# Performance work log

Hardware: AMD Instinct MI355X
Metric: run time of the kernel (lower is better)

Reference implementation:

```python
import jax, jax.numpy as jnp
import numpy as np

N, C, W_DIM, H_DIM = 2, 256, 64, 64
HEADS = 4
DH = C // HEADS  # per-head dim for Q,K,V projections
EPS = 1e-5


def _layernorm(x, w, b):
    mu = jnp.mean(x, axis=-1, keepdims=True)
    var = jnp.var(x, axis=-1, keepdims=True)
    return (x - mu) * jax.lax.rsqrt(var + EPS) * w + b


def setup_inputs() -> dict:
    key = jax.random.key(0)
    ks = jax.random.split(key, 12)
    s = 1.0 / np.sqrt(C)
    return {
        "x": jax.random.normal(ks[0], (N, C, W_DIM, H_DIM), dtype=jnp.float32),
        "ln1_w": jnp.ones((C,), jnp.float32),
        "ln1_b": jnp.zeros((C,), jnp.float32),
        # per-head projection weights, laid out for x @ W: [heads, C, DH]
        "WQ": jax.random.normal(ks[1], (HEADS, C, DH), jnp.float32) * s,
        "WK": jax.random.normal(ks[2], (HEADS, C, DH), jnp.float32) * s,
        "WV": jax.random.normal(ks[3], (HEADS, C, DH), jnp.float32) * s,
        "ln2_w": jnp.ones((C,), jnp.float32),
        "ln2_b": jnp.zeros((C,), jnp.float32),
        "W1": jax.random.normal(ks[4], (C, C), jnp.float32) * s,
        "b1": jnp.zeros((C,), jnp.float32),
        "W2": jax.random.normal(ks[5], (C, C), jnp.float32) * s,
        "b2": jnp.zeros((C,), jnp.float32),
    }


def reference(x, ln1_w, ln1_b, WQ, WK, WV, ln2_w, ln2_b, W1, b1, W2, b2):
    n, c, w, h = x.shape
    s = w * h
    # 'n c w h -> n (w h) c'
    r = x.reshape(n, c, s).transpose(0, 2, 1)          # [n, s, c]
    norm = _layernorm(r, ln1_w, ln1_b)
    # all heads at once (original loops over heads)
    Q = jnp.einsum('nsc,hcd->nhsd', norm, WQ)
    K = jnp.einsum('nsc,hcd->nhsd', norm, WK)
    V = jnp.einsum('nsc,hcd->nhsd', norm, WV)
    # scale is 1/sqrt(seq_len) per original (keys.shape[1])
    y = jnp.einsum('nhqd,nhkd->nhqk', Q, K) / jnp.sqrt(jnp.float32(s))
    # QUIRK: softmax over dim=1 of [n, q, k] => the QUERY axis (axis=2 here)
    z = jax.nn.softmax(y, axis=2)
    attn = jnp.einsum('nhqk,nhkd->nhqd', z, V)         # [n, h, s, dh]
    attn_cat = attn.transpose(0, 2, 1, 3).reshape(n, s, c)
    out = attn_cat + r
    out = _layernorm(out, ln2_w, ln2_b)
    out = jax.nn.gelu(out @ W1 + b1, approximate=False) @ W2 + b2
    out = out + attn_cat
    # 'n (w h) c -> n c w h'
    return out.transpose(0, 2, 1).reshape(n, c, w, h)
```

## Files before the change

### kernel.cpp

```cpp
#include <hip/hip_runtime.h>
#include <math.h>

#define SEQ 4096
#define CH  256
#define NHT 8
#define DHD 64

#define QSCALE 0.0225421092f

using bf16x8 = __attribute__((ext_vector_type(8))) short;
using f32x4  = __attribute__((ext_vector_type(4))) float;
typedef unsigned short u16;
typedef unsigned int   u32;

__device__ __forceinline__ u16 f2bf(float f) {
    u32 u = __float_as_uint(f);
    u = (u + 0x7fffu + ((u >> 16) & 1u)) >> 16;
    return (u16)u;
}
__device__ __forceinline__ float bf2f(u16 h) {
    return __uint_as_float(((u32)h) << 16);
}
__device__ __forceinline__ float fexp2(float x) {
    return __builtin_amdgcn_exp2f(x);
}

__global__ __launch_bounds__(256) void k_prep(const float* __restrict__ x,
                                              const float* __restrict__ ln1w,
                                              const float* __restrict__ ln1b,
                                              const float* __restrict__ WQ,
                                              const float* __restrict__ WK,
                                              const float* __restrict__ WV,
                                              const float* __restrict__ W1,
                                              const float* __restrict__ W2,
                                              u16* __restrict__ norm,
                                              u16* __restrict__ BtQKV,
                                              u16* __restrict__ W1t,
                                              u16* __restrict__ W2t)
{
    __shared__ float tile[32][257];
    __shared__ float mu[32], rs[32];
    int bid = blockIdx.x;
    int t = threadIdx.x;
    if (bid < 1280) {
        int id = bid * 256 + t;
        if (id < 768 * 256) {
            int j = id >> 8, c = id & 255;
            int which = j >> 8, h = (j >> 6) & 3, d = j & 63;
            const float* W = (which == 0) ? WQ : (which == 1) ? WK : WV;
            BtQKV[id] = f2bf(W[(h * 256 + c) * 64 + d]);
        } else if (id < 768 * 256 + 65536) {
            int jj = id - 768 * 256;
            int j = jj >> 8, c = jj & 255;
            W1t[jj] = f2bf(W1[c * 256 + j]);
        } else if (id < 768 * 256 + 2 * 65536) {
            int jj = id - 768 * 256 - 65536;
            int j = jj >> 8, c = jj & 255;
            W2t[jj] = f2bf(W2[c * 256 + j]);
        }
        return;
    }
    int b2i = bid - 1280;
    int n = b2i >> 7, s0 = (b2i & 127) * 32;
    int sl = t & 31, cg = t >> 5;
    for (int cc = 0; cc < 256; cc += 8) {
        int c = cc + cg;
        tile[sl][c] = x[(n * 256 + c) * SEQ + s0 + sl];
    }
    __syncthreads();
    int wv = t >> 6, l = t & 63;
    for (int rr = 0; rr < 8; rr++) {
        int s = wv * 8 + rr;
        float a0 = tile[s][l], a1 = tile[s][l + 64], a2 = tile[s][l + 128], a3 = tile[s][l + 192];
        float sm = a0 + a1 + a2 + a3;
        float sq = a0 * a0 + a1 * a1 + a2 * a2 + a3 * a3;
        for (int off = 32; off; off >>= 1) { sm += __shfl_xor(sm, off); sq += __shfl_xor(sq, off); }
        if (l == 0) {
            float m = sm * (1.f / 256.f);
            mu[s] = m;
            rs[s] = rsqrtf(sq * (1.f / 256.f) - m * m + 1e-5f);
        }
    }
    __syncthreads();
    float ww = ln1w[t], bb = ln1b[t];
    for (int s = 0; s < 32; s++) {
        float v = (tile[s][t] - mu[s]) * rs[s] * ww + bb;
        norm[(n * SEQ + s0 + s) * 256 + t] = f2bf(v);
    }
}

__global__ __launch_bounds__(256) void k_qkv(const u16* __restrict__ norm,
                                             const u16* __restrict__ Bt,
                                             u16* __restrict__ Qo,
                                             u16* __restrict__ Ko,
                                             u16* __restrict__ Vo)
{
    int m0 = blockIdx.x * 64, j0 = blockIdx.y * 128;
    int t = threadIdx.x, w = t >> 6, lane = t & 63, quad = lane >> 4, l16 = lane & 15;
    const u16* Ap = norm + (long)(m0 + w * 16 + l16) * 256;
    const u16* Bp = Bt + (long)j0 * 256;
    f32x4 z = {0.f, 0.f, 0.f, 0.f};
    f32x4 acc[8];
    #pragma unroll
    for (int j = 0; j < 8; j++) acc[j] = z;
    #pragma unroll
    for (int kc = 0; kc < 8; kc++) {
        bf16x8 a = *(const bf16x8*)&Ap[kc * 32 + quad * 8];
        #pragma unroll
        for (int j = 0; j < 8; j++) {
            bf16x8 b = *(const bf16x8*)&Bp[(long)(j * 16 + l16) * 256 + kc * 32 + quad * 8];
            acc[j] = __builtin_amdgcn_mfma_f32_16x16x32_bf16(a, b, acc[j], 0, 0, 0);
        }
    }
    #pragma unroll
    for (int j = 0; j < 8; j++) {
        int col = j0 + j * 16 + l16;
        int which = col >> 8, h = (col >> 6) & 3, d = col & 63;
        u16* dst = (which == 0) ? Qo : (which == 1) ? Ko : Vo;
        float sc = (which == 0) ? QSCALE : 1.0f;
        #pragma unroll
        for (int r = 0; r < 4; r++) {
            int m = m0 + w * 16 + quad * 4 + r;
            int n = m >> 12, s = m & 4095;
            dst[((n * 4 + h) * SEQ + s) * 64 + d] = f2bf(acc[j][r] * sc);
        }
    }
}

__global__ __launch_bounds__(256) void k_pass1(const u16* __restrict__ Q,
                                               const u16* __restrict__ Km,
                                               float* __restrict__ D4)
{
    __shared__ float Dred[128];
    int nh = blockIdx.y, k0 = blockIdx.x * 128, qc = blockIdx.z;
    const u16* Qh = Q + (long)nh * SEQ * 64;
    const u16* Kh = Km + (long)nh * SEQ * 64;
    int t = threadIdx.x, w = t >> 6, lane = t & 63, quad = lane >> 4, l16 = lane & 15;
    bf16x8 Kf[8][2];
    #pragma unroll
    for (int i = 0; i < 8; i++) {
        Kf[i][0] = *(const bf16x8*)&Kh[(k0 + i * 16 + l16) * 64 + quad * 8];
        Kf[i][1] = *(const bf16x8*)&Kh[(k0 + i * 16 + l16) * 64 + 32 + quad * 8];
    }
    if (t < 128) Dred[t] = 0.f;
    f32x4 z = {0.f, 0.f, 0.f, 0.f};
    float Dacc[8][4] = {};
    const int qw0 = qc * 1024 + w * 256;
    bf16x8 b0 = *(const bf16x8*)&Qh[(qw0 + l16) * 64 + quad * 8];
    bf16x8 b1 = *(const bf16x8*)&Qh[(qw0 + l16) * 64 + 32 + quad * 8];
    for (int step = 0; step < 16; step++) {
        int q = qw0 + step * 16;
        bf16x8 n0, n1;
        if (step < 15) {
            n0 = *(const bf16x8*)&Qh[(q + 16 + l16) * 64 + quad * 8];
            n1 = *(const bf16x8*)&Qh[(q + 16 + l16) * 64 + 32 + quad * 8];
        }
        #pragma unroll
        for (int i = 0; i < 8; i++) {
            f32x4 acc = z;
            acc = __builtin_amdgcn_mfma_f32_16x16x32_bf16(Kf[i][0], b0, acc, 0, 0, 0);
            acc = __builtin_amdgcn_mfma_f32_16x16x32_bf16(Kf[i][1], b1, acc, 0, 0, 0);
            #pragma unroll
            for (int r = 0; r < 4; r++) Dacc[i][r] += fexp2(acc[r]);
        }
        b0 = n0; b1 = n1;
    }
    #pragma unroll
    for (int i = 0; i < 8; i++)
        #pragma unroll
        for (int r = 0; r < 4; r++) {
            float v = Dacc[i][r];
            v += __shfl_xor(v, 1); v += __shfl_xor(v, 2);
            v += __shfl_xor(v, 4); v += __shfl_xor(v, 8);
            Dacc[i][r] = v;
        }
    __syncthreads();
    if (l16 == 0) {
        #pragma unroll
        for (int i = 0; i < 8; i++)
            #pragma unroll
            for (int r = 0; r < 4; r++)
                atomicAdd(&Dred[i * 16 + quad * 4 + r], Dacc[i][r]);
    }
    __syncthreads();
    if (t < 128) D4[((long)(qc * NHT + nh)) * SEQ + k0 + t] = Dred[t];
}

__global__ __launch_bounds__(256) void k_scaleV(const u16* __restrict__ V,
                                                const float* __restrict__ D4,
                                                u16* __restrict__ Vt)
{
    __shared__ float tile[64][65];
    int nh = blockIdx.y, k0 = blockIdx.x * 64;
    int t = threadIdx.x;
    int d = t & 63, kk = t >> 6;
    const u16* Vh = V + (long)nh * SEQ * 64;
    for (int p = 0; p < 16; p++) {
        int k = p * 4 + kk;
        float Dv = D4[((long)(0 * NHT + nh)) * SEQ + k0 + k]
                 + D4[((long)(1 * NHT + nh)) * SEQ + k0 + k]
                 + D4[((long)(2 * NHT + nh)) * SEQ + k0 + k]
                 + D4[((long)(3 * NHT + nh)) * SEQ + k0 + k];
        tile[k][d] = bf2f(Vh[(k0 + k) * 64 + d]) * (1.f / Dv);
    }
    __syncthreads();
    int k2 = t & 63, d4 = t >> 6;
    u16* Vth = Vt + (long)nh * 64 * SEQ;
    for (int p = 0; p < 16; p++) {
        int dd = p * 4 + d4;
        Vth[dd * SEQ + k0 + k2] = f2bf(tile[k2][dd]);
    }
}

__global__ __launch_bounds__(256) void k_pass2(const u16* __restrict__ Q,
                                               const u16* __restrict__ Km,
                                               const u16* __restrict__ Vt,
                                               float* __restrict__ acat2)
{
    __shared__ __align__(16) unsigned char smem[34816];
    u16 (*lP)[64][36] = (u16(*)[64][36])smem;
    float (*SA)[68] = (float(*)[68])smem;
    float (*SB)[68] = (float(*)[68])(smem + 17408);

    int nh = blockIdx.y, q0 = blockIdx.x * 64, kcid = blockIdx.z;
    int n = nh >> 2, h = nh & 3;
    const u16* Qh = Q + (long)nh * SEQ * 64;
    const u16* Kh = Km + (long)nh * SEQ * 64;
    const u16* Vh = Vt + (long)nh * 64 * SEQ;
    int t = threadIdx.x, w = t >> 6, lane = t & 63, quad = lane >> 4, l16 = lane & 15;
    bf16x8 Qf[4][2];
    #pragma unroll
    for (int jq = 0; jq < 4; jq++)
        #pragma unroll
        for (int ch = 0; ch < 2; ch++)
            Qf[jq][ch] = *(const bf16x8*)&Qh[(q0 + jq * 16 + l16) * 64 + ch * 32 + quad * 8];
    f32x4 z = {0.f, 0.f, 0.f, 0.f};
    f32x4 accO[4][4];
    #pragma unroll
    for (int jq = 0; jq < 4; jq++)
        #pragma unroll
        for (int jd = 0; jd < 4; jd++) accO[jq][jd] = z;

    const int kw0 = kcid * 2048 + w * 512;
    bf16x8 kA[2][2], nA[2][2];
    #pragma unroll
    for (int ksub = 0; ksub < 2; ksub++) {
        kA[ksub][0] = *(const bf16x8*)&Kh[(kw0 + ksub * 16 + l16) * 64 + quad * 8];
        kA[ksub][1] = *(const bf16x8*)&Kh[(kw0 + ksub * 16 + l16) * 64 + 32 + quad * 8];
    }
    for (int step = 0; step < 16; step++) {
        int k0 = kw0 + step * 32;
        if (step < 15) {
            #pragma unroll
            for (int ksub = 0; ksub < 2; ksub++) {
                nA[ksub][0] = *(const bf16x8*)&Kh[(k0 + 32 + ksub * 16 + l16) * 64 + quad * 8];
                nA[ksub][1] = *(const bf16x8*)&Kh[(k0 + 32 + ksub * 16 + l16) * 64 + 32 + quad * 8];
            }
        }
        #pragma unroll
        for (int ksub = 0; ksub < 2; ksub++) {
            #pragma unroll
            for (int jq = 0; jq < 4; jq++) {
                f32x4 acc = z;
                acc = __builtin_amdgcn_mfma_f32_16x16x32_bf16(kA[ksub][0], Qf[jq][0], acc, 0, 0, 0);
                acc = __builtin_amdgcn_mfma_f32_16x16x32_bf16(kA[ksub][1], Qf[jq][1], acc, 0, 0, 0);
                u32 e0 = __float_as_uint(fexp2(acc[0]));
                u32 e1 = __float_as_uint(fexp2(acc[1]));
                u32 e2 = __float_as_uint(fexp2(acc[2]));
                u32 e3 = __float_as_uint(fexp2(acc[3]));
                uint2 pk;
                pk.x = __builtin_amdgcn_perm(e1, e0, 0x07060302u);
                pk.y = __builtin_amdgcn_perm(e3, e2, 0x07060302u);
                *(uint2*)&lP[w][jq * 16 + l16][ksub * 16 + quad * 4] = pk;
            }
        }
        #pragma unroll
        for (int jq = 0; jq < 4; jq++) {
            bf16x8 pa = *(const bf16x8*)&lP[w][jq * 16 + l16][quad * 8];
            #pragma unroll
            for (int jd = 0; jd < 4; jd++) {
                bf16x8 vb = *(const bf16x8*)&Vh[(jd * 16 + l16) * SEQ + k0 + quad * 8];
                accO[jq][jd] = __builtin_amdgcn_mfma_f32_16x16x32_bf16(pa, vb, accO[jq][jd], 0, 0, 0);
            }
        }
        #pragma unroll
        for (int ksub = 0; ksub < 2; ksub++) {
            kA[ksub][0] = nA[ksub][0];
            kA[ksub][1] = nA[ksub][1];
        }
    }
    __syncthreads();
    if (w >= 2) {
        float (*S)[68] = (w == 2) ? SA : SB;
        #pragma unroll
        for (int jq = 0; jq < 4; jq++)
            #pragma unroll
            for (int jd = 0; jd < 4; jd++)
                #pragma unroll
                for (int r = 0; r < 4; r++)
                    S[jq * 16 + quad * 4 + r][jd * 16 + l16] = accO[jq][jd][r];
    }
    __syncthreads();
    if (w < 2) {
        float (*S)[68] = (w == 0) ? SA : SB;
        #pragma unroll
        for (int jq = 0; jq < 4; jq++)
            #pragma unroll
            for (int jd = 0; jd < 4; jd++)
                #pragma unroll
                for (int r = 0; r < 4; r++) {
                    float v = accO[jq][jd][r] + S[jq * 16 + quad * 4 + r][jd * 16 + l16];
                    S[jq * 16 + quad * 4 + r][jd * 16 + l16] = v;
                }
    }
    __syncthreads();
    float* dst = acat2 + (long)kcid * 8192 * 256;
    #pragma unroll
    for (int p = 0; p < 4; p++) {
        int row = p * 16 + (t >> 4);
        int ch = (t & 15) * 4;
        float4 va = *(float4*)&SA[row][ch];
        float4 vb = *(float4*)&SB[row][ch];
        float4 o = make_float4(va.x + vb.x, va.y + vb.y, va.z + vb.z, va.w + vb.w);
        *(float4*)&dst[((long)n * SEQ + q0 + row) * 256 + h * 64 + ch] = o;
    }
}

__global__ __launch_bounds__(256) void k_tail(const float* __restrict__ x,
                                              const float* __restrict__ acat2,
                                              const float* __restrict__ lnw,
                                              const float* __restrict__ lnb,
                                              const u16* __restrict__ W1t,
                                              const float* __restrict__ b1v,
                                              const u16* __restrict__ W2t,
                                              const float* __restrict__ b2v,
                                              float* __restrict__ out)
{
    __shared__ __align__(16) unsigned char smem[16448];
    float (*tile)[257] = (float(*)[257])smem;
    u16 (*lT)[264] = (u16(*)[264])smem;
    __shared__ float mu[16], rs[16];
    __shared__ __align__(16) u16 lH[16][264];

    const long STRIDE = (long)8192 * 256;
    int m0 = blockIdx.x * 16;
    int n = m0 >> 12, s0 = m0 & 4095;
    int t = threadIdx.x, w = t >> 6, lane = t & 63, quad = lane >> 4, l16 = lane & 15;

    {
        int sl = t & 15, cg = t >> 4;
        for (int cc = 0; cc < 256; cc += 16) {
            int c = cc + cg;
            tile[sl][c] = x[(n * 256 + c) * SEQ + s0 + sl];
        }
    }
    __syncthreads();
    for (int s = 0; s < 16; s++) {
        long idx = (long)(m0 + s) * 256 + t;
        tile[s][t] += acat2[idx] + acat2[idx + STRIDE];
    }
    __syncthreads();
    {
        int l = t & 63;
        for (int rr = 0; rr < 4; rr++) {
            int s = w * 4 + rr;
            float a0 = tile[s][l], a1 = tile[s][l + 64], a2 = tile[s][l + 128], a3 = tile[s][l + 192];
            float sm = a0 + a1 + a2 + a3;
            float sq = a0 * a0 + a1 * a1 + a2 * a2 + a3 * a3;
            for (int off = 32; off; off >>= 1) { sm += __shfl_xor(sm, off); sq += __shfl_xor(sq, off); }
            if (l == 0) {
                float m = sm * (1.f / 256.f);
                mu[s] = m;
                rs[s] = rsqrtf(sq * (1.f / 256.f) - m * m + 1e-5f);
            }
        }
    }
    __syncthreads();
    {
        float ww = lnw[t], bb = lnb[t];
        for (int s = 0; s < 16; s++)
            lH[s][t] = f2bf((tile[s][t] - mu[s]) * rs[s] * ww + bb);
    }
    __syncthreads();

    f32x4 z = {0.f, 0.f, 0.f, 0.f};
    f32x4 acc1[4];
    #pragma unroll
    for (int js = 0; js < 4; js++) acc1[js] = z;
    #pragma unroll
    for (int kc = 0; kc < 8; kc++) {
        bf16x8 b = *(const bf16x8*)&lH[l16][kc * 32 + quad * 8];
        #pragma unroll
        for (int js = 0; js < 4; js++) {
            bf16x8 a = *(const bf16x8*)&W1t[(long)(w * 64 + js * 16 + l16) * 256 + kc * 32 + quad * 8];
            acc1[js] = __builtin_amdgcn_mfma_f32_16x16x32_bf16(a, b, acc1[js], 0, 0, 0);
        }
    }
    #pragma unroll
    for (int js = 0; js < 4; js++) {
        u32 e[4];
        #pragma unroll
        for (int r = 0; r < 4; r++) {
            int j = w * 64 + js * 16 + quad * 4 + r;
            float v = acc1[js][r] + b1v[j];
            float g = 0.5f * v * (1.f + erff(v * 0.70710678118f));
            u32 u = __float_as_uint(g);
            e[r] = u + 0x7fffu + ((u >> 16) & 1u);
        }
        uint2 pk;
        pk.x = __builtin_amdgcn_perm(e[1], e[0], 0x07060302u);
        pk.y = __builtin_amdgcn_perm(e[3], e[2], 0x07060302u);
        *(uint2*)&lT[l16][w * 64 + js * 16 + quad * 4] = pk;
    }
    __syncthreads();
    f32x4 acc2[4];
    #pragma unroll
    for (int cs = 0; cs < 4; cs++) acc2[cs] = z;
    #pragma unroll
    for (int kc = 0; kc < 8; kc++) {
        bf16x8 pa = *(const bf16x8*)&lT[l16][kc * 32 + quad * 8];
        #pragma unroll
        for (int cs = 0; cs < 4; cs++) {
            bf16x8 wb = *(const bf16x8*)&W2t[(long)(w * 64 + cs * 16 + l16) * 256 + kc * 32 + quad * 8];
            acc2[cs] = __builtin_amdgcn_mfma_f32_16x16x32_bf16(pa, wb, acc2[cs], 0, 0, 0);
        }
    }
    #pragma unroll
    for (int cs = 0; cs < 4; cs++) {
        int c = w * 64 + cs * 16 + l16;
        float bj = b2v[c];
        float vv[4];
        #pragma unroll
        for (int r = 0; r < 4; r++) {
            long idx = (long)(m0 + quad * 4 + r) * 256 + c;
            vv[r] = acc2[cs][r] + bj + acat2[idx] + acat2[idx + STRIDE];
        }
        float4 o = make_float4(vv[0], vv[1], vv[2], vv[3]);
        *(float4*)&out[((long)n * 256 + c) * SEQ + s0 + quad * 4] = o;
    }
}

extern "C" void kernel_launch(void* const* d_in, const int* in_sizes, int n_in,
                              void* d_out, int out_size, void* d_ws, size_t ws_size,
                              hipStream_t stream) {
    const float* x    = (const float*)d_in[0];
    const float* ln1w = (const float*)d_in[1];
    const float* ln1b = (const float*)d_in[2];
    const float* WQ   = (const float*)d_in[3];
    const float* WK   = (const float*)d_in[4];
    const float* WV   = (const float*)d_in[5];
    const float* ln2w = (const float*)d_in[6];
    const float* ln2b = (const float*)d_in[7];
    const float* W1   = (const float*)d_in[8];
    const float* b1   = (const float*)d_in[9];
    const float* W2   = (const float*)d_in[10];
    const float* b2   = (const float*)d_in[11];
    float* out = (float*)d_out;

    char* p = (char*)d_ws;
    u16* norm   = (u16*)p;   p += (size_t)8192 * 256 * 2;
    u16* BtQKV  = (u16*)p;   p += (size_t)768 * 256 * 2;
    u16* W1t    = (u16*)p;   p += (size_t)256 * 256 * 2;
    u16* W2t    = (u16*)p;   p += (size_t)256 * 256 * 2;
    u16* Qb     = (u16*)p;   p += (size_t)NHT * SEQ * 64 * 2;
    u16* Kb     = (u16*)p;   p += (size_t)NHT * SEQ * 64 * 2;
    u16* Vb     = (u16*)p;   p += (size_t)NHT * SEQ * 64 * 2;
    float* D4   = (float*)p; p += (size_t)4 * NHT * SEQ * 4;
    u16* Vt     = (u16*)p;   p += (size_t)NHT * SEQ * 64 * 2;
    float* acat2= (float*)p; p += (size_t)2 * 8192 * 256 * 4;

    k_prep<<<1536, 256, 0, stream>>>(x, ln1w, ln1b, WQ, WK, WV, W1, W2,
                                     norm, BtQKV, W1t, W2t);
    k_qkv<<<dim3(128, 6), 256, 0, stream>>>(norm, BtQKV, Qb, Kb, Vb);
    k_pass1<<<dim3(32, 8, 4), 256, 0, stream>>>(Qb, Kb, D4);
    k_scaleV<<<dim3(64, 8), 256, 0, stream>>>(Vb, D4, Vt);
    k_pass2<<<dim3(64, 8, 2), 256, 0, stream>>>(Qb, Kb, Vt, acat2);
    k_tail<<<512, 256, 0, stream>>>(x, acat2, ln2w, ln2b, W1t, b1, W2t, b2, out);
}
```

Before: 257.6 us.

## Fold softmax normalization into pass2 exponent and write V transposed from QKV

Removes the k_scaleV kernel. The QKV GEMM now writes V directly in transposed [d][seq] layout. pass2 loads the per-key column sums into LDS as log2 values and subtracts them inside the exponent, so the normalization no longer multiplies V. pass2 is also restructured to software-pipeline the QK exponentials into registers one step ahead and to prefetch the V fragments. The aim is to save a kernel launch and a full read/write of V. The cost is extra LDS traffic and register pressure in pass2, and the change in rounding (bf16 V no longer pre-scaled).

```diff
diff --git a/kernel.cpp b/kernel.cpp
--- a/kernel.cpp
+++ b/kernel.cpp
@@ -93,7 +93,7 @@
                                              const u16* __restrict__ Bt,
                                              u16* __restrict__ Qo,
                                              u16* __restrict__ Ko,
-                                             u16* __restrict__ Vo)
+                                             u16* __restrict__ Vto)
 {
     int m0 = blockIdx.x * 64, j0 = blockIdx.y * 128;
     int t = threadIdx.x, w = t >> 6, lane = t & 63, quad = lane >> 4, l16 = lane & 15;
@@ -116,13 +116,21 @@
     for (int j = 0; j < 8; j++) {
         int col = j0 + j * 16 + l16;
         int which = col >> 8, h = (col >> 6) & 3, d = col & 63;
-        u16* dst = (which == 0) ? Qo : (which == 1) ? Ko : Vo;
-        float sc = (which == 0) ? QSCALE : 1.0f;
-        #pragma unroll
-        for (int r = 0; r < 4; r++) {
-            int m = m0 + w * 16 + quad * 4 + r;
-            int n = m >> 12, s = m & 4095;
-            dst[((n * 4 + h) * SEQ + s) * 64 + d] = f2bf(acc[j][r] * sc);
+        int m = m0 + w * 16 + quad * 4;
+        int n = m >> 12, s = m & 4095;
+        if (which == 2) {
+            u16 h0 = f2bf(acc[j][0]), h1 = f2bf(acc[j][1]);
+            u16 h2_ = f2bf(acc[j][2]), h3 = f2bf(acc[j][3]);
+            uint2 pk;
+            pk.x = (u32)h0 | ((u32)h1 << 16);
+            pk.y = (u32)h2_ | ((u32)h3 << 16);
+            *(uint2*)&Vto[((long)(n * 4 + h) * 64 + d) * SEQ + s] = pk;
+        } else {
+            u16* dst = (which == 0) ? Qo : Ko;
+            float sc = (which == 0) ? QSCALE : 1.0f;
+            #pragma unroll
+            for (int r = 0; r < 4; r++)
+                dst[((n * 4 + h) * SEQ + s + r) * 64 + d] = f2bf(acc[j][r] * sc);
         }
     }
 }
@@ -186,39 +194,15 @@
     if (t < 128) D4[((long)(qc * NHT + nh)) * SEQ + k0 + t] = Dred[t];
 }
 
-__global__ __launch_bounds__(256) void k_scaleV(const u16* __restrict__ V,
-                                                const float* __restrict__ D4,
-                                                u16* __restrict__ Vt)
-{
-    __shared__ float tile[64][65];
-    int nh = blockIdx.y, k0 = blockIdx.x * 64;
-    int t = threadIdx.x;
-    int d = t & 63, kk = t >> 6;
-    const u16* Vh = V + (long)nh * SEQ * 64;
-    for (int p = 0; p < 16; p++) {
-        int k = p * 4 + kk;
-        float Dv = D4[((long)(0 * NHT + nh)) * SEQ + k0 + k]
-                 + D4[((long)(1 * NHT + nh)) * SEQ + k0 + k]
-                 + D4[((long)(2 * NHT + nh)) * SEQ + k0 + k]
-                 + D4[((long)(3 * NHT + nh)) * SEQ + k0 + k];
-        tile[k][d] = bf2f(Vh[(k0 + k) * 64 + d]) * (1.f / Dv);
-    }
-    __syncthreads();
-    int k2 = t & 63, d4 = t >> 6;
-    u16* Vth = Vt + (long)nh * 64 * SEQ;
-    for (int p = 0; p < 16; p++) {
-        int dd = p * 4 + d4;
-        Vth[dd * SEQ + k0 + k2] = f2bf(tile[k2][dd]);
-    }
-}
-
 __global__ __launch_bounds__(256) void k_pass2(const u16* __restrict__ Q,
                                                const u16* __restrict__ Km,
                                                const u16* __restrict__ Vt,
+                                               const float* __restrict__ D4,
                                                float* __restrict__ acat2)
 {
     __shared__ __align__(16) unsigned char smem[34816];
     u16 (*lP)[64][36] = (u16(*)[64][36])smem;
+    float* Lk = (float*)(smem + 18432);
     float (*SA)[68] = (float(*)[68])smem;
     float (*SB)[68] = (float(*)[68])(smem + 17408);
 
@@ -228,65 +212,115 @@
     const u16* Kh = Km + (long)nh * SEQ * 64;
     const u16* Vh = Vt + (long)nh * 64 * SEQ;
     int t = threadIdx.x, w = t >> 6, lane = t & 63, quad = lane >> 4, l16 = lane & 15;
+    const int kw0 = kcid * 2048 + w * 512;
+    const int klw = w * 512;
+
+    {
+        const float* Dp = D4 + (long)nh * SEQ + kcid * 2048;
+        const long QS = (long)NHT * SEQ;
+        #pragma unroll
+        for (int off = 0; off < 8; off++) {
+            int kl = off * 256 + t;
+            float s = Dp[kl] + Dp[QS + kl] + Dp[2 * QS + kl] + Dp[3 * QS + kl];
+            Lk[kl] = __log2f(s);
+        }
+    }
     bf16x8 Qf[4][2];
     #pragma unroll
     for (int jq = 0; jq < 4; jq++)
         #pragma unroll
         for (int ch = 0; ch < 2; ch++)
             Qf[jq][ch] = *(const bf16x8*)&Qh[(q0 + jq * 16 + l16) * 64 + ch * 32 + quad * 8];
-    f32x4 z = {0.f, 0.f, 0.f, 0.f};
-    f32x4 accO[4][4];
-    #pragma unroll
-    for (int jq = 0; jq < 4; jq++)
-        #pragma unroll
-        for (int jd = 0; jd < 4; jd++) accO[jq][jd] = z;
-
-    const int kw0 = kcid * 2048 + w * 512;
-    bf16x8 kA[2][2], nA[2][2];
+    bf16x8 kA[2][2];
     #pragma unroll
     for (int ksub = 0; ksub < 2; ksub++) {
         kA[ksub][0] = *(const bf16x8*)&Kh[(kw0 + ksub * 16 + l16) * 64 + quad * 8];
         kA[ksub][1] = *(const bf16x8*)&Kh[(kw0 + ksub * 16 + l16) * 64 + 32 + quad * 8];
     }
-    for (int step = 0; step < 16; step++) {
-        int k0 = kw0 + step * 32;
-        if (step < 15) {
-            #pragma unroll
-            for (int ksub = 0; ksub < 2; ksub++) {
-                nA[ksub][0] = *(const bf16x8*)&Kh[(k0 + 32 + ksub * 16 + l16) * 64 + quad * 8];
-                nA[ksub][1] = *(const bf16x8*)&Kh[(k0 + 32 + ksub * 16 + l16) * 64 + 32 + quad * 8];
-            }
-        }
-        #pragma unroll
-        for (int ksub = 0; ksub < 2; ksub++) {
+    f32x4 z = {0.f, 0.f, 0.f, 0.f};
+    f32x4 accO[4][4];
+    #pragma unroll
+    for (int jq = 0; jq < 4; jq++)
+        #pragma unroll
+        for (int jd = 0; jd < 4; jd++) accO[jq][jd] = z;
+    __syncthreads();
+
+    uint2 pk[2][4];
+    {
+        f32x4 Lv[2];
+        #pragma unroll
+        for (int ksub = 0; ksub < 2; ksub++)
+            Lv[ksub] = *(const f32x4*)&Lk[klw + ksub * 16 + quad * 4];
+        #pragma unroll
+        for (int ksub = 0; ksub < 2; ksub++)
             #pragma unroll
             for (int jq = 0; jq < 4; jq++) {
                 f32x4 acc = z;
                 acc = __builtin_amdgcn_mfma_f32_16x16x32_bf16(kA[ksub][0], Qf[jq][0], acc, 0, 0, 0);
                 acc = __builtin_amdgcn_mfma_f32_16x16x32_bf16(kA[ksub][1], Qf[jq][1], acc, 0, 0, 0);
-                u32 e0 = __float_as_uint(fexp2(acc[0]));
-                u32 e1 = __float_as_uint(fexp2(acc[1]));
-                u32 e2 = __float_as_uint(fexp2(acc[2]));
-                u32 e3 = __float_as_uint(fexp2(acc[3]));
-                uint2 pk;
-                pk.x = __builtin_amdgcn_perm(e1, e0, 0x07060302u);
-                pk.y = __builtin_amdgcn_perm(e3, e2, 0x07060302u);
-                *(uint2*)&lP[w][jq * 16 + l16][ksub * 16 + quad * 4] = pk;
+                u32 e0 = __float_as_uint(fexp2(acc[0] - Lv[ksub][0]));
+                u32 e1 = __float_as_uint(fexp2(acc[1] - Lv[ksub][1]));
+                u32 e2 = __float_as_uint(fexp2(acc[2] - Lv[ksub][2]));
+                u32 e3 = __float_as_uint(fexp2(acc[3] - Lv[ksub][3]));
+                pk[ksub][jq].x = __builtin_amdgcn_perm(e1, e0, 0x07060302u);
+                pk[ksub][jq].y = __builtin_amdgcn_perm(e3, e2, 0x07060302u);
+            }
+    }
+    #pragma unroll
+    for (int ksub = 0; ksub < 2; ksub++) {
+        kA[ksub][0] = *(const bf16x8*)&Kh[(kw0 + 32 + ksub * 16 + l16) * 64 + quad * 8];
+        kA[ksub][1] = *(const bf16x8*)&Kh[(kw0 + 32 + ksub * 16 + l16) * 64 + 32 + quad * 8];
+    }
+    bf16x8 vb[4];
+    #pragma unroll
+    for (int jd = 0; jd < 4; jd++)
+        vb[jd] = *(const bf16x8*)&Vh[(jd * 16 + l16) * SEQ + kw0 + quad * 8];
+
+    for (int i = 0; i < 16; i++) {
+        int k0 = kw0 + i * 32;
+        #pragma unroll
+        for (int ksub = 0; ksub < 2; ksub++)
+            #pragma unroll
+            for (int jq = 0; jq < 4; jq++)
+                *(uint2*)&lP[w][jq * 16 + l16][ksub * 16 + quad * 4] = pk[ksub][jq];
+        if (i < 15) {
+            f32x4 Lv[2];
+            #pragma unroll
+            for (int ksub = 0; ksub < 2; ksub++)
+                Lv[ksub] = *(const f32x4*)&Lk[klw + (i + 1) * 32 + ksub * 16 + quad * 4];
+            #pragma unroll
+            for (int ksub = 0; ksub < 2; ksub++)
+                #pragma unroll
+                for (int jq = 0; jq < 4; jq++) {
+                    f32x4 acc = z;
+                    acc = __builtin_amdgcn_mfma_f32_16x16x32_bf16(kA[ksub][0], Qf[jq][0], acc, 0, 0, 0);
+                    acc = __builtin_amdgcn_mfma_f32_16x16x32_bf16(kA[ksub][1], Qf[jq][1], acc, 0, 0, 0);
+                    u32 e0 = __float_as_uint(fexp2(acc[0] - Lv[ksub][0]));
+                    u32 e1 = __float_as_uint(fexp2(acc[1] - Lv[ksub][1]));
+                    u32 e2 = __float_as_uint(fexp2(acc[2] - Lv[ksub][2]));
+                    u32 e3 = __float_as_uint(fexp2(acc[3] - Lv[ksub][3]));
+                    pk[ksub][jq].x = __builtin_amdgcn_perm(e1, e0, 0x07060302u);
+                    pk[ksub][jq].y = __builtin_amdgcn_perm(e3, e2, 0x07060302u);
+                }
+            if (i < 14) {
+                #pragma unroll
+                for (int ksub = 0; ksub < 2; ksub++) {
+                    kA[ksub][0] = *(const bf16x8*)&Kh[(k0 + 64 + ksub * 16 + l16) * 64 + quad * 8];
+                    kA[ksub][1] = *(const bf16x8*)&Kh[(k0 + 64 + ksub * 16 + l16) * 64 + 32 + quad * 8];
+                }
             }
         }
         #pragma unroll
         for (int jq = 0; jq < 4; jq++) {
             bf16x8 pa = *(const bf16x8*)&lP[w][jq * 16 + l16][quad * 8];
             #pragma unroll
-            for (int jd = 0; jd < 4; jd++) {
-                bf16x8 vb = *(const bf16x8*)&Vh[(jd * 16 + l16) * SEQ + k0 + quad * 8];
-                accO[jq][jd] = __builtin_amdgcn_mfma_f32_16x16x32_bf16(pa, vb, accO[jq][jd], 0, 0, 0);
-            }
-        }
-        #pragma unroll
-        for (int ksub = 0; ksub < 2; ksub++) {
-            kA[ksub][0] = nA[ksub][0];
-            kA[ksub][1] = nA[ksub][1];
+            for (int jd = 0; jd < 4; jd++)
+                accO[jq][jd] = __builtin_amdgcn_mfma_f32_16x16x32_bf16(pa, vb[jd], accO[jq][jd], 0, 0, 0);
+        }
+        if (i < 15) {
+            #pragma unroll
+            for (int jd = 0; jd < 4; jd++)
+                vb[jd] = *(const bf16x8*)&Vh[(jd * 16 + l16) * SEQ + k0 + 32 + quad * 8];
         }
     }
     __syncthreads();
@@ -320,8 +354,8 @@
         int row = p * 16 + (t >> 4);
         int ch = (t & 15) * 4;
         float4 va = *(float4*)&SA[row][ch];
-        float4 vb = *(float4*)&SB[row][ch];
-        float4 o = make_float4(va.x + vb.x, va.y + vb.y, va.z + vb.z, va.w + vb.w);
+        float4 vb2 = *(float4*)&SB[row][ch];
+        float4 o = make_float4(va.x + vb2.x, va.y + vb2.y, va.z + vb2.z, va.w + vb2.w);
         *(float4*)&dst[((long)n * SEQ + q0 + row) * 256 + h * 64 + ch] = o;
     }
 }
@@ -464,16 +498,14 @@
     u16* W2t    = (u16*)p;   p += (size_t)256 * 256 * 2;
     u16* Qb     = (u16*)p;   p += (size_t)NHT * SEQ * 64 * 2;
     u16* Kb     = (u16*)p;   p += (size_t)NHT * SEQ * 64 * 2;
-    u16* Vb     = (u16*)p;   p += (size_t)NHT * SEQ * 64 * 2;
+    u16* VtT    = (u16*)p;   p += (size_t)NHT * SEQ * 64 * 2;
     float* D4   = (float*)p; p += (size_t)4 * NHT * SEQ * 4;
-    u16* Vt     = (u16*)p;   p += (size_t)NHT * SEQ * 64 * 2;
     float* acat2= (float*)p; p += (size_t)2 * 8192 * 256 * 4;
 
     k_prep<<<1536, 256, 0, stream>>>(x, ln1w, ln1b, WQ, WK, WV, W1, W2,
                                      norm, BtQKV, W1t, W2t);
-    k_qkv<<<dim3(128, 6), 256, 0, stream>>>(norm, BtQKV, Qb, Kb, Vb);
+    k_qkv<<<dim3(128, 6), 256, 0, stream>>>(norm, BtQKV, Qb, Kb, VtT);
     k_pass1<<<dim3(32, 8, 4), 256, 0, stream>>>(Qb, Kb, D4);
-    k_scaleV<<<dim3(64, 8), 256, 0, stream>>>(Vb, D4, Vt);
-    k_pass2<<<dim3(64, 8, 2), 256, 0, stream>>>(Qb, Kb, Vt, acat2);
+    k_pass2<<<dim3(64, 8, 2), 256, 0, stream>>>(Qb, Kb, VtT, D4, acat2);
     k_tail<<<512, 256, 0, stream>>>(x, acat2, ln2w, ln2b, W1t, b1, W2t, b2, out);
 }
```

New measurement: 243.3 us. 5.6% less time.
